# Optimization experiments

Measured on AMD Instinct MI355X. Metric: run time of the kernel, lower is better.

Reference implementation:

```python
import jax, jax.numpy as jnp
import numpy as np

B = 512
IN_CORES = 12      # input_eff_capsules = 3072/256
N_PRIM = 12        # num_primary_capsules
N_PAR = 10         # num_parent_capsules
RFPC = 4           # receptive fields per capsule = 256/64
RF = 64            # receptive field size
CAP = 256          # capsule size
P_CONN = 0.2


def setup_inputs() -> dict:
    key = jax.random.key(0)
    ks = jax.random.split(key, 16)
    x = jax.random.uniform(ks[0], (B, 32, 32, 3), dtype=jnp.float32)
    # sparse 0/1 routing tensors (fixed Bernoulli(p) connectivity, stored as float params)
    C1 = jax.random.bernoulli(ks[1], P_CONN, (IN_CORES, RFPC, N_PRIM, RFPC)).astype(jnp.float32)
    C_skip = jax.random.bernoulli(ks[2], P_CONN, (IN_CORES, RFPC, N_PAR, RFPC)).astype(jnp.float32)
    C2 = jax.random.bernoulli(ks[3], P_CONN, (N_PRIM, RFPC, N_PAR, RFPC)).astype(jnp.float32)
    # per-receptive-field linear weights of the capsule layers
    s = 1.0 / np.sqrt(RF)
    W1 = jax.random.normal(ks[4], (N_PRIM, RFPC, RF, RF), dtype=jnp.float32) * s
    b1 = jnp.zeros((N_PRIM, RFPC, RF), dtype=jnp.float32)
    W2 = jax.random.normal(ks[5], (N_PAR, RFPC, RF, RF), dtype=jnp.float32) * s
    b2 = jnp.zeros((N_PAR, RFPC, RF), dtype=jnp.float32)
    # reconstruction MLP: 2560 -> 5000 -> 4000 -> 3072
    Wr1 = jax.random.normal(ks[6], (2560, 5000), dtype=jnp.float32) * (1.0 / np.sqrt(2560))
    br1 = jnp.zeros((5000,), dtype=jnp.float32)
    Wr2 = jax.random.normal(ks[7], (5000, 4000), dtype=jnp.float32) * (1.0 / np.sqrt(5000))
    br2 = jnp.zeros((4000,), dtype=jnp.float32)
    Wr3 = jax.random.normal(ks[8], (4000, 3072), dtype=jnp.float32) * (1.0 / np.sqrt(4000))
    br3 = jnp.zeros((3072,), dtype=jnp.float32)
    return {"x": x, "C1": C1, "W1": W1, "b1": b1, "C_skip": C_skip,
            "C2": C2, "W2": W2, "b2": b2,
            "Wr1": Wr1, "br1": br1, "Wr2": Wr2, "br2": br2, "Wr3": Wr3, "br3": br3}


def _caps_layer(x_flat, C, W, b):
    # x_flat: (B, in_cores*RFPC*RF); C: (in_cores, RFPC, out_caps, RFPC)
    bsz = x_flat.shape[0]
    in_cores = C.shape[0]
    xr = x_flat.reshape(bsz, in_cores, RFPC, RF)
    routed = jnp.einsum('ijkl,bijm->bklm', C, xr)          # (B, out_caps, RFPC, RF)
    out = jax.nn.relu(jnp.einsum('bklm,klmn->bkln', routed, W) + b)
    return out.reshape(bsz, -1)


def reference(x, C1, W1, b1, C_skip, C2, W2, b2, Wr1, br1, Wr2, br2, Wr3, br3):
    bsz = x.shape[0]
    # spatial_block_reshape: pure reshapes -> flatten
    x_flat = x.reshape(bsz, -1)                             # (B, 3072)
    # primary capsule layer
    x_prim = _caps_layer(x_flat, C1, W1, b1)                # (B, 3072)
    # skip connection: sparse routing einsum input->parent
    xr = x_prim.reshape(bsz, IN_CORES, RFPC, RF)
    x_skip = jnp.einsum('ijkl,bijm->bklm', C_skip, xr).reshape(bsz, -1)  # (B, 2560)
    # parent capsule layer + skip
    x_sum = x_skip + _caps_layer(x_prim, C2, W2, b2)        # (B, 2560)
    # top-1 capsule mask by norm
    norms = jnp.linalg.norm(x_sum.reshape(bsz, N_PAR, CAP), axis=-1)  # (B, 10)
    active = jnp.argmax(norms, axis=-1)                     # (B,)
    cap_id = jnp.arange(N_PAR * CAP) // CAP                 # (2560,)
    mask = (cap_id[None, :] == active[:, None]).astype(x_sum.dtype)
    x_recon = mask * x_sum
    # reconstruction MLP
    h = jax.nn.relu(x_recon @ Wr1 + br1)
    h = jax.nn.relu(h @ Wr2 + br2)
    out = jax.nn.sigmoid(h @ Wr3 + br3)                     # (B, 3072)
    return (out, x_sum)
```

## Files before the change

kernel.cpp:

```cpp
#include <hip/hip_runtime.h>
#include <math.h>


#define BATCH 512
#define OUT0_SZ (512*3072)

#define KP1 2576
#define KP2 5136
#define KP3 4112
#define LD_XREC 2576
#define LD_H1 5136
#define LD_H2 4112
#define LDP2 4224
#define LDP3 3200
#define SPLITK 4

typedef __attribute__((ext_vector_type(8))) short short8;
typedef __attribute__((ext_vector_type(4))) float f32x4;

__device__ inline unsigned short f2bf(float f) {
    union { float f; unsigned u; } v; v.f = f;
    unsigned r = v.u + 0x7fffu + ((v.u >> 16) & 1u);
    return (unsigned short)(r >> 16);
}
__device__ inline float bf2f(unsigned int hi16) {
    union { unsigned u; float f; } v; v.u = hi16 << 16; return v.f;
}

#define GLD16(g, l) __builtin_amdgcn_global_load_lds( \
    (const __attribute__((address_space(1))) unsigned int*)(g), \
    (__attribute__((address_space(3))) unsigned int*)(l), 16, 0, 0)

#define GUEST_SMEM 16640

#define CONV_PARAMS const float* __restrict__ cWr1, unsigned short* __restrict__ cWt1, \
    const float* __restrict__ cWr2, unsigned short* __restrict__ cWt2, \
    const float* __restrict__ cWr3, unsigned short* __restrict__ cWt3

__device__ void conv_guest(int t, char* smem, CONV_PARAMS)
{
    float* sh = (float*)smem;
    const float* W; unsigned short* Wt;
    int Kr, Nr, Kp, ktiles, rem;
    if (t < 3200)      { W = cWr1; Wt = cWt1; Kr = 2560; Nr = 5000; Kp = KP1; ktiles = 40; rem = t; }
    else if (t < 8320) { W = cWr2; Wt = cWt2; Kr = 5000; Nr = 4000; Kp = KP2; ktiles = 80; rem = t - 3200; }
    else               { W = cWr3; Wt = cWt3; Kr = 4000; Nr = 3072; Kp = KP3; ktiles = 64; rem = t - 8320; }
    int k0 = (rem % ktiles) * 64;
    int n0 = (rem / ktiles) * 64;
    int tid = threadIdx.x;

    {
        int kr = tid >> 4;
        int nc = (tid & 15) * 4;
        #pragma unroll
        for (int p = 0; p < 4; ++p) {
            int k = k0 + kr + p * 16;
            float4 v = make_float4(0.f, 0.f, 0.f, 0.f);
            if (k < Kr) {
                if (n0 + nc + 3 < Nr) {
                    v = *(const float4*)&W[(size_t)k * Nr + n0 + nc];
                } else {
                    float tmp[4] = {0.f, 0.f, 0.f, 0.f};
                    #pragma unroll
                    for (int j = 0; j < 4; ++j)
                        if (n0 + nc + j < Nr) tmp[j] = W[(size_t)k * Nr + n0 + nc + j];
                    v = make_float4(tmp[0], tmp[1], tmp[2], tmp[3]);
                }
            }
            float* row = &sh[(kr + p * 16) * 65 + nc];
            row[0] = v.x; row[1] = v.y; row[2] = v.z; row[3] = v.w;
        }
    }
    __syncthreads();
    {
        int nr = tid >> 2;
        int kc = (tid & 3) * 16;
        unsigned int u[8];
        #pragma unroll
        for (int j = 0; j < 8; ++j) {
            float v0 = sh[(kc + 2 * j)     * 65 + nr];
            float v1 = sh[(kc + 2 * j + 1) * 65 + nr];
            u[j] = (unsigned int)f2bf(v0) | ((unsigned int)f2bf(v1) << 16);
        }
        unsigned int* dst = (unsigned int*)&Wt[(size_t)(n0 + nr) * Kp + k0 + kc];
        *(uint4*)(dst)     = make_uint4(u[0], u[1], u[2], u[3]);
        *(uint4*)(dst + 4) = make_uint4(u[4], u[5], u[6], u[7]);
    }
}

__global__ __launch_bounds__(256) void conv_small(
    const float* __restrict__ W1, unsigned short* __restrict__ W1t,
    const float* __restrict__ W2, unsigned short* __restrict__ W2t)
{
    __shared__ __align__(16) float sh[64 * 65];
    int bid = blockIdx.x;
    const float* W; unsigned short* Wt;
    if (bid < 48) { W = W1 + (size_t)bid * 4096; Wt = W1t + (size_t)bid * 4096; }
    else          { W = W2 + (size_t)(bid - 48) * 4096; Wt = W2t + (size_t)(bid - 48) * 4096; }
    int tid = threadIdx.x;
    int kr = tid >> 4, nc = (tid & 15) * 4;
    #pragma unroll
    for (int p = 0; p < 4; ++p) {
        float4 v = *(const float4*)&W[(size_t)(kr + p * 16) * 64 + nc];
        float* row = &sh[(kr + p * 16) * 65 + nc];
        row[0] = v.x; row[1] = v.y; row[2] = v.z; row[3] = v.w;
    }
    __syncthreads();
    int nr = tid >> 2, kc = (tid & 3) * 16;
    unsigned int u[8];
    #pragma unroll
    for (int j = 0; j < 8; ++j) {
        float v0 = sh[(kc + 2 * j)     * 65 + nr];
        float v1 = sh[(kc + 2 * j + 1) * 65 + nr];
        u[j] = (unsigned int)f2bf(v0) | ((unsigned int)f2bf(v1) << 16);
    }
    unsigned int* dst = (unsigned int*)&Wt[(size_t)nr * 64 + kc];
    *(uint4*)(dst)     = make_uint4(u[0], u[1], u[2], u[3]);
    *(uint4*)(dst + 4) = make_uint4(u[4], u[5], u[6], u[7]);
}

__global__ __launch_bounds__(256) void caps_gemm1_f(
    const float* __restrict__ x, const float* __restrict__ C1,
    const unsigned short* __restrict__ W1t, const float* __restrict__ b1,
    unsigned short* __restrict__ xp, int hostBlocks, int guestBase,
    CONV_PARAMS)
{
    __shared__ __align__(16) char smem[27840];
    if ((int)blockIdx.x >= hostBlocks) {
        conv_guest(guestBase + blockIdx.x - hostBlocks, smem, cWr1, cWt1, cWr2, cWt2, cWr3, cWt3);
        return;
    }
    unsigned short* As = (unsigned short*)smem;
    unsigned short* Bs = (unsigned short*)(smem + 18432);
    float* Csh = (float*)(smem + 27648);

    int kl = blockIdx.x % 48;
    int bm = (blockIdx.x / 48) * 128;
    int tid = threadIdx.x;
    int w = tid >> 6, lane = tid & 63, q = lane >> 4, r16 = lane & 15;
    int wm = (w >> 1) * 64, wn = (w & 1) * 32;

    if (tid < 48) Csh[tid] = C1[tid * 48 + kl];
    {
        const uint4* src = (const uint4*)(W1t + (size_t)kl * 4096);
        #pragma unroll
        for (int p = 0; p < 2; ++p) {
            int c = tid + p * 256;
            int row = c >> 3, cq = c & 7;
            *(uint4*)&Bs[row * 72 + cq * 8] = src[c];
        }
    }
    __syncthreads();

    int arow = tid >> 1, ah = (tid & 1) * 32;
    float accp[32];
    #pragma unroll
    for (int i = 0; i < 32; ++i) accp[i] = 0.f;
    const float* xrow = x + (size_t)(bm + arow) * 3072 + ah;
    for (int ij = 0; ij < 48; ++ij) {
        float c = Csh[ij];
        if (c != 0.f) {
            const float4* p4 = (const float4*)(xrow + ij * 64);
            #pragma unroll
            for (int cc = 0; cc < 8; ++cc) {
                float4 v = p4[cc];
                accp[cc * 4 + 0] = fmaf(c, v.x, accp[cc * 4 + 0]);
                accp[cc * 4 + 1] = fmaf(c, v.y, accp[cc * 4 + 1]);
                accp[cc * 4 + 2] = fmaf(c, v.z, accp[cc * 4 + 2]);
                accp[cc * 4 + 3] = fmaf(c, v.w, accp[cc * 4 + 3]);
            }
        }
    }
    {
        unsigned short* dst = &As[arow * 72 + ah];
        #pragma unroll
        for (int cc = 0; cc < 4; ++cc) {
            unsigned int u[4];
            #pragma unroll
            for (int j = 0; j < 4; ++j)
                u[j] = (unsigned int)f2bf(accp[cc * 8 + 2 * j]) |
                       ((unsigned int)f2bf(accp[cc * 8 + 2 * j + 1]) << 16);
            *(uint4*)&dst[cc * 8] = make_uint4(u[0], u[1], u[2], u[3]);
        }
    }
    __syncthreads();

    f32x4 acc[4][2];
    #pragma unroll
    for (int i = 0; i < 4; ++i)
        #pragma unroll
        for (int j = 0; j < 2; ++j) acc[i][j] = (f32x4)0.f;
    #pragma unroll
    for (int ks = 0; ks < 2; ++ks) {
        short8 a[4], b[2];
        #pragma unroll
        for (int mt = 0; mt < 4; ++mt)
            a[mt] = *(const short8*)&As[(wm + mt * 16 + r16) * 72 + ks * 32 + q * 8];
        #pragma unroll
        for (int nt = 0; nt < 2; ++nt)
            b[nt] = *(const short8*)&Bs[(wn + nt * 16 + r16) * 72 + ks * 32 + q * 8];
        #pragma unroll
        for (int mt = 0; mt < 4; ++mt)
            #pragma unroll
            for (int nt = 0; nt < 2; ++nt)
                acc[mt][nt] = __builtin_amdgcn_mfma_f32_16x16x32_bf16(a[mt], b[nt], acc[mt][nt], 0, 0, 0);
    }

    #pragma unroll
    for (int mt = 0; mt < 4; ++mt) {
        #pragma unroll
        for (int nt = 0; nt < 2; ++nt) {
            int n = wn + nt * 16 + r16;
            float bv = b1[kl * 64 + n];
            #pragma unroll
            for (int reg = 0; reg < 4; ++reg) {
                int row = bm + wm + mt * 16 + q * 4 + reg;
                xp[(size_t)row * 3072 + kl * 64 + n] = f2bf(fmaxf(acc[mt][nt][reg] + bv, 0.f));
            }
        }
    }
}

__global__ __launch_bounds__(256) void caps_gemm2_f(
    const unsigned short* __restrict__ xp, const float* __restrict__ Cs,
    const float* __restrict__ C2, const unsigned short* __restrict__ W2t,
    const float* __restrict__ b2, float* __restrict__ xsum,
    float* __restrict__ part8, int hostBlocks, int guestBase,
    CONV_PARAMS)
{
    __shared__ __align__(16) char smem[28032];
    if ((int)blockIdx.x >= hostBlocks) {
        conv_guest(guestBase + blockIdx.x - hostBlocks, smem, cWr1, cWt1, cWr2, cWt2, cWr3, cWt3);
        return;
    }
    unsigned short* As = (unsigned short*)smem;
    unsigned short* Bs = (unsigned short*)(smem + 18432);
    float* C2sh = (float*)(smem + 27648);
    float* Cssh = (float*)(smem + 27840);

    int kl = blockIdx.x % 40;
    int bm = (blockIdx.x / 40) * 128;
    int tid = threadIdx.x;
    int w = tid >> 6, lane = tid & 63, q = lane >> 4, r16 = lane & 15;
    int wm = (w >> 1) * 64, wn = (w & 1) * 32;
    int half = w & 1;

    if (tid < 48) { C2sh[tid] = C2[tid * 40 + kl]; Cssh[tid] = Cs[tid * 40 + kl]; }
    {
        const uint4* src = (const uint4*)(W2t + (size_t)kl * 4096);
        #pragma unroll
        for (int p = 0; p < 2; ++p) {
            int c = tid + p * 256;
            int row = c >> 3, cq = c & 7;
            *(uint4*)&Bs[row * 72 + cq * 8] = src[c];
        }
    }
    __syncthreads();

    int arow = tid >> 1, ah = (tid & 1) * 32;
    float accp[32], skp[32];
    #pragma unroll
    for (int i = 0; i < 32; ++i) { accp[i] = 0.f; skp[i] = 0.f; }
    const unsigned short* xprow = xp + (size_t)(bm + arow) * 3072 + ah;
    for (int ij = 0; ij < 48; ++ij) {
        float c2 = C2sh[ij], cs = Cssh[ij];
        if (c2 != 0.f || cs != 0.f) {
            const uint4* p4 = (const uint4*)(xprow + ij * 64);
            #pragma unroll
            for (int cc = 0; cc < 4; ++cc) {
                uint4 v = p4[cc];
                unsigned int uu[4] = {v.x, v.y, v.z, v.w};
                #pragma unroll
                for (int j = 0; j < 4; ++j) {
                    float lo = bf2f(uu[j] & 0xffffu);
                    float hi = bf2f(uu[j] >> 16);
                    int idx = cc * 8 + 2 * j;
                    accp[idx]     = fmaf(c2, lo, accp[idx]);
                    accp[idx + 1] = fmaf(c2, hi, accp[idx + 1]);
                    skp[idx]      = fmaf(cs, lo, skp[idx]);
                    skp[idx + 1]  = fmaf(cs, hi, skp[idx + 1]);
                }
            }
        }
    }
    {
        unsigned short* dst = &As[arow * 72 + ah];
        #pragma unroll
        for (int cc = 0; cc < 4; ++cc) {
            unsigned int u[4];
            #pragma unroll
            for (int j = 0; j < 4; ++j)
                u[j] = (unsigned int)f2bf(accp[cc * 8 + 2 * j]) |
                       ((unsigned int)f2bf(accp[cc * 8 + 2 * j + 1]) << 16);
            *(uint4*)&dst[cc * 8] = make_uint4(u[0], u[1], u[2], u[3]);
        }
        float* sx = xsum + (size_t)(bm + arow) * 2560 + kl * 64 + ah;
        #pragma unroll
        for (int cc = 0; cc < 8; ++cc)
            *(float4*)&sx[cc * 4] = make_float4(skp[cc*4], skp[cc*4+1], skp[cc*4+2], skp[cc*4+3]);
    }
    __syncthreads();

    f32x4 acc[4][2];
    #pragma unroll
    for (int i = 0; i < 4; ++i)
        #pragma unroll
        for (int j = 0; j < 2; ++j) acc[i][j] = (f32x4)0.f;
    #pragma unroll
    for (int ks = 0; ks < 2; ++ks) {
        short8 a[4], b[2];
        #pragma unroll
        for (int mt = 0; mt < 4; ++mt)
            a[mt] = *(const short8*)&As[(wm + mt * 16 + r16) * 72 + ks * 32 + q * 8];
        #pragma unroll
        for (int nt = 0; nt < 2; ++nt)
            b[nt] = *(const short8*)&Bs[(wn + nt * 16 + r16) * 72 + ks * 32 + q * 8];
        #pragma unroll
        for (int mt = 0; mt < 4; ++mt)
            #pragma unroll
            for (int nt = 0; nt < 2; ++nt)
                acc[mt][nt] = __builtin_amdgcn_mfma_f32_16x16x32_bf16(a[mt], b[nt], acc[mt][nt], 0, 0, 0);
    }

    #pragma unroll
    for (int mt = 0; mt < 4; ++mt) {
        float sreg[4] = {0.f, 0.f, 0.f, 0.f};
        #pragma unroll
        for (int nt = 0; nt < 2; ++nt) {
            int n = wn + nt * 16 + r16;
            float bv = b2[kl * 64 + n];
            #pragma unroll
            for (int reg = 0; reg < 4; ++reg) {
                int lr = wm + mt * 16 + q * 4 + reg;
                size_t xi = (size_t)(bm + lr) * 2560 + kl * 64 + n;
                float v = xsum[xi] + fmaxf(acc[mt][nt][reg] + bv, 0.f);
                xsum[xi] = v;
                sreg[reg] += v * v;
            }
        }
        #pragma unroll
        for (int reg = 0; reg < 4; ++reg) {
            float s = sreg[reg];
            s += __shfl_xor(s, 1); s += __shfl_xor(s, 2);
            s += __shfl_xor(s, 4); s += __shfl_xor(s, 8);
            if (r16 == 0) {
                int row = bm + wm + mt * 16 + q * 4 + reg;
                part8[(size_t)row * 80 + kl * 2 + half] = s;
            }
        }
    }
}

__global__ __launch_bounds__(256) void mask_f(
    const float* __restrict__ xs, const float* __restrict__ part8,
    unsigned short* __restrict__ xrec, int* __restrict__ active,
    int hostBlocks, int guestBase, CONV_PARAMS)
{
    __shared__ __align__(16) char smem[GUEST_SMEM + 64];
    if ((int)blockIdx.x >= hostBlocks) {
        conv_guest(guestBase + blockIdx.x - hostBlocks, smem, cWr1, cWt1, cWr2, cWt2, cWr3, cWt3);
        return;
    }
    float* norms = (float*)smem;
    int* actp = (int*)(smem + 40);
    int b = blockIdx.x;
    int tid = threadIdx.x;
    if (tid < 10) {
        float s = 0.f;
        #pragma unroll
        for (int j = 0; j < 8; ++j) s += part8[(size_t)b * 80 + tid * 8 + j];
        norms[tid] = s;
    }
    __syncthreads();
    if (tid == 0) {
        int best = 0; float bn = -1.f;
        #pragma unroll
        for (int k = 0; k < 10; ++k)
            if (norms[k] > bn) { bn = norms[k]; best = k; }
        *actp = best;
        active[b] = best;
    }
    __syncthreads();
    int act = *actp;
    int idx = act * 256 + tid;
    xrec[(size_t)b * LD_XREC + idx] = f2bf(xs[(size_t)b * 2560 + idx]);
}

__global__ __launch_bounds__(256) void bucket_f(
    const int* __restrict__ active, int* __restrict__ perm,
    int4* __restrict__ slots, int hostBlocks, int guestBase, CONV_PARAMS)
{
    __shared__ __align__(16) char smem[GUEST_SMEM + 128];
    if ((int)blockIdx.x >= hostBlocks) {
        conv_guest(guestBase + blockIdx.x - hostBlocks, smem, cWr1, cWt1, cWr2, cWt2, cWr3, cWt3);
        return;
    }
    int* cnt = (int*)smem;
    int* pos = cnt + 10;
    int tid = threadIdx.x;
    if (tid < 10) cnt[tid] = 0;
    __syncthreads();
    int a0 = active[tid], a1 = active[tid + 256];
    atomicAdd(&cnt[a0], 1);
    atomicAdd(&cnt[a1], 1);
    __syncthreads();
    if (tid == 0) {
        int o = 0, s = 0;
        for (int g = 0; g < 10; ++g) {
            pos[g] = o;
            int mg = cnt[g];
            for (int t0 = 0; t0 < mg; t0 += 64)
                slots[s++] = make_int4(g, o + t0, min(64, mg - t0), 0);
            o += mg;
        }
        for (; s < 18; ++s) slots[s] = make_int4(0, 0, 0, 0);
    }
    __syncthreads();
    int r0 = atomicAdd(&pos[a0], 1);
    perm[r0] = tid;
    int r1 = atomicAdd(&pos[a1], 1);
    perm[r1] = tid + 256;
}

__global__ __launch_bounds__(256) void gemm_l1_f(
    const unsigned short* __restrict__ xrec, const int* __restrict__ perm,
    const int4* __restrict__ slots, const unsigned short* __restrict__ Wt1,
    const float* __restrict__ br1, unsigned short* __restrict__ h1,
    int hostBlocks, int guestBase, CONV_PARAMS)
{
    __shared__ __align__(16) char smem[GUEST_SMEM];
    if ((int)blockIdx.x >= hostBlocks) {
        conv_guest(guestBase + blockIdx.x - hostBlocks, smem, cWr1, cWt1, cWr2, cWt2, cWr3, cWt3);
        return;
    }
    unsigned short* As = (unsigned short*)smem;
    unsigned short* Bs = (unsigned short*)(smem + 4096);
    int* rows = (int*)(smem + 12288);

    int sy = blockIdx.x % 18;
    int bn = (blockIdx.x / 18) * 128;
    int4 s = slots[sy];
    if (s.z == 0) return;
    int g = s.x, mstart = s.y, mval = s.z;
    int tid = threadIdx.x;

    if (tid < 64) rows[tid] = perm[mstart + min(tid, mval - 1)];
    __syncthreads();

    int w = tid >> 6, lane = tid & 63;
    int wm = (w >> 1) * 32, wn = (w & 1) * 64;
    int q = lane >> 4, r16 = lane & 15;
    int srow = tid >> 2, skq = tid & 3;

    f32x4 acc[2][4];
    #pragma unroll
    for (int i = 0; i < 2; ++i)
        #pragma unroll
        for (int j = 0; j < 4; ++j) acc[i][j] = (f32x4)0.f;

    int arow = rows[srow];
    const unsigned short* ga = xrec + (size_t)arow * LD_XREC + g * 256 + skq * 8;
    const unsigned short* gb = Wt1 + (size_t)(bn + srow) * KP1 + g * 256 + skq * 8;

    for (int kk = 0; kk < 256; kk += 32) {
        GLD16(ga + kk, &As[tid * 8]);
        GLD16(gb + kk, &Bs[tid * 8]);
        GLD16(gb + kk + (size_t)64 * KP1, &Bs[(tid + 256) * 8]);
        __syncthreads();

        short8 a[2], b[4];
        #pragma unroll
        for (int mt = 0; mt < 2; ++mt)
            a[mt] = *(const short8*)&As[(wm + mt * 16 + r16) * 32 + q * 8];
        #pragma unroll
        for (int nt = 0; nt < 4; ++nt)
            b[nt] = *(const short8*)&Bs[(wn + nt * 16 + r16) * 32 + q * 8];
        #pragma unroll
        for (int mt = 0; mt < 2; ++mt)
            #pragma unroll
            for (int nt = 0; nt < 4; ++nt)
                acc[mt][nt] = __builtin_amdgcn_mfma_f32_16x16x32_bf16(a[mt], b[nt], acc[mt][nt], 0, 0, 0);
        __syncthreads();
    }

    #pragma unroll
    for (int mt = 0; mt < 2; ++mt) {
        #pragma unroll
        for (int nt = 0; nt < 4; ++nt) {
            int n = bn + wn + nt * 16 + r16;
            float bv = (n < 5000) ? br1[n] : 0.f;
            #pragma unroll
            for (int reg = 0; reg < 4; ++reg) {
                int lm = wm + mt * 16 + q * 4 + reg;
                if (lm < mval)
                    h1[(size_t)(mstart + lm) * LD_H1 + n] =
                        f2bf(fmaxf(acc[mt][nt][reg] + bv, 0.f));
            }
        }
    }
}

__global__ __launch_bounds__(256) void gemm_splitk_f(
    const unsigned short* __restrict__ A, int ldA,
    const unsigned short* __restrict__ Bt, int ldB,
    float* __restrict__ P, int ldP, int Np, int kper, int nbx,
    int hostBlocks, int guestBase, CONV_PARAMS)
{
    __shared__ __align__(16) char smem[GUEST_SMEM];
    if ((int)blockIdx.x >= hostBlocks) {
        conv_guest(guestBase + blockIdx.x - hostBlocks, smem, cWr1, cWt1, cWr2, cWt2, cWr3, cWt3);
        return;
    }
    unsigned short* As = (unsigned short*)smem;
    unsigned short* Bs = (unsigned short*)(smem + 4096);

    int tid = threadIdx.x;
    int bid = blockIdx.x;
    int bn = (bid % nbx) * 128;
    int bm = ((bid / nbx) & 7) * 64;
    int z  = bid / (nbx * 8);
    int kz = z * kper;

    int w = tid >> 6, lane = tid & 63;
    int wm = (w >> 1) * 32, wn = (w & 1) * 64;
    int q = lane >> 4, r16 = lane & 15;
    int srow = tid >> 2, skq = tid & 3;

    f32x4 acc[2][4];
    #pragma unroll
    for (int i = 0; i < 2; ++i)
        #pragma unroll
        for (int j = 0; j < 4; ++j) acc[i][j] = (f32x4)0.f;

    for (int kk = 0; kk < kper; kk += 32) {
        int k0 = kz + kk;
        const unsigned short* ga = A + (size_t)(bm + srow) * ldA + k0 + skq * 8;
        GLD16(ga, &As[tid * 8]);
        const unsigned short* gb = Bt + (size_t)(bn + srow) * ldB + k0 + skq * 8;
        GLD16(gb, &Bs[tid * 8]);
        GLD16(gb + (size_t)64 * ldB, &Bs[(tid + 256) * 8]);
        __syncthreads();

        short8 a[2], b[4];
        #pragma unroll
        for (int mt = 0; mt < 2; ++mt)
            a[mt] = *(const short8*)&As[(wm + mt * 16 + r16) * 32 + q * 8];
        #pragma unroll
        for (int nt = 0; nt < 4; ++nt)
            b[nt] = *(const short8*)&Bs[(wn + nt * 16 + r16) * 32 + q * 8];
        #pragma unroll
        for (int mt = 0; mt < 2; ++mt)
            #pragma unroll
            for (int nt = 0; nt < 4; ++nt)
                acc[mt][nt] = __builtin_amdgcn_mfma_f32_16x16x32_bf16(a[mt], b[nt], acc[mt][nt], 0, 0, 0);
        __syncthreads();
    }

    float* Pz = P + (size_t)z * 512 * ldP;
    #pragma unroll
    for (int mt = 0; mt < 2; ++mt) {
        #pragma unroll
        for (int nt = 0; nt < 4; ++nt) {
            int cn = bn + wn + nt * 16 + r16;
            #pragma unroll
            for (int reg = 0; reg < 4; ++reg) {
                int cm = bm + wm + mt * 16 + q * 4 + reg;
                Pz[(size_t)cm * ldP + cn] = acc[mt][nt][reg];
            }
        }
    }
}

template<int MODE>
__global__ __launch_bounds__(256) void combine_f(
    const float* __restrict__ P, int ldP, const float* __restrict__ bias,
    void* __restrict__ out, int ldO, int Np, int N_real,
    const int* __restrict__ perm, int hostBlocks, int guestBase, CONV_PARAMS)
{
    __shared__ __align__(16) char smem[GUEST_SMEM];
    if ((int)blockIdx.x >= hostBlocks) {
        conv_guest(guestBase + blockIdx.x - hostBlocks, smem, cWr1, cWt1, cWr2, cWt2, cWr3, cWt3);
        return;
    }
    int gid = blockIdx.x * 256 + threadIdx.x;
    int n0 = (gid * 4) % Np;
    int m  = (gid * 4) / Np;
    size_t MN = (size_t)512 * ldP;
    const float* p = P + (size_t)m * ldP + n0;
    f32x4 s = *(const f32x4*)p;
    s += *(const f32x4*)(p + MN);
    s += *(const f32x4*)(p + 2 * MN);
    s += *(const f32x4*)(p + 3 * MN);
    f32x4 bv = (n0 < N_real) ? *(const f32x4*)(bias + n0) : (f32x4)0.f;
    s += bv;
    if (MODE == 0) {
        unsigned int lo = (unsigned int)f2bf(fmaxf(s[0], 0.f)) | ((unsigned int)f2bf(fmaxf(s[1], 0.f)) << 16);
        unsigned int hi = (unsigned int)f2bf(fmaxf(s[2], 0.f)) | ((unsigned int)f2bf(fmaxf(s[3], 0.f)) << 16);
        *(uint2*)((unsigned short*)out + (size_t)m * ldO + n0) = make_uint2(lo, hi);
    } else {
        int row = perm[m];
        f32x4 v;
        v[0] = 1.f / (1.f + expf(-s[0]));
        v[1] = 1.f / (1.f + expf(-s[1]));
        v[2] = 1.f / (1.f + expf(-s[2]));
        v[3] = 1.f / (1.f + expf(-s[3]));
        *(f32x4*)((float*)out + (size_t)row * ldO + n0) = v;
    }
}

extern "C" void kernel_launch(void* const* d_in, const int* in_sizes, int n_in,
                              void* d_out, int out_size, void* d_ws, size_t ws_size,
                              hipStream_t stream) {
    const float* x   = (const float*)d_in[0];
    const float* C1  = (const float*)d_in[1];
    const float* W1  = (const float*)d_in[2];
    const float* b1  = (const float*)d_in[3];
    const float* Cs  = (const float*)d_in[4];
    const float* C2  = (const float*)d_in[5];
    const float* W2  = (const float*)d_in[6];
    const float* b2  = (const float*)d_in[7];
    const float* Wr1 = (const float*)d_in[8];
    const float* br1 = (const float*)d_in[9];
    const float* Wr2 = (const float*)d_in[10];
    const float* br2 = (const float*)d_in[11];
    const float* Wr3 = (const float*)d_in[12];
    const float* br3 = (const float*)d_in[13];

    float* out = (float*)d_out;
    float* out0     = out;
    float* xsum_out = out + OUT0_SZ;

    char* base = (char*)d_ws;
    unsigned short* xrec = (unsigned short*)(base);
    unsigned short* h1   = (unsigned short*)(base +   2637824);
    unsigned short* h2   = (unsigned short*)(base +   7897088);
    unsigned short* Wt1  = (unsigned short*)(base +  12107776);
    unsigned short* Wt2  = (unsigned short*)(base +  38486016);
    unsigned short* Wt3  = (unsigned short*)(base +  80560128);
    float*          Pbuf = (float*)(base + 105824256);
    unsigned short* xp   = (unsigned short*)(base + 140427264);
    unsigned short* W1t  = (unsigned short*)(base + 143572992);
    unsigned short* W2t  = (unsigned short*)(base + 143966208);
    float*          part8= (float*)(base + 144293888);
    int*  active = (int*)(base + 144457728);
    int*  perm   = active + 512;
    int4* slots  = (int4*)(perm + 512);

    #define CARGS Wr1, Wt1, Wr2, Wt2, Wr3, Wt3

    conv_small<<<88, 256, 0, stream>>>(W1, W1t, W2, W2t);

    caps_gemm1_f<<<192 + 1600, 256, 0, stream>>>(x, C1, W1t, b1, xp, 192, 0, CARGS);
    caps_gemm2_f<<<160 + 1600, 256, 0, stream>>>(xp, Cs, C2, W2t, b2, xsum_out, part8, 160, 1600, CARGS);
    mask_f<<<512 + 1300, 256, 0, stream>>>(xsum_out, part8, xrec, active, 512, 3200, CARGS);
    bucket_f<<<1 + 1300, 256, 0, stream>>>(active, perm, slots, 1, 4500, CARGS);

    gemm_l1_f<<<720 + 2520, 256, 0, stream>>>(xrec, perm, slots, Wt1, br1, h1, 720, 5800, CARGS);

    gemm_splitk_f<<<1024 + 2000, 256, 0, stream>>>(h1, LD_H1, Wt2, KP2, Pbuf, LDP2, 4096, 5120 / SPLITK, 32, 1024, 8320, CARGS);
    combine_f<0><<<2048 + 1072, 256, 0, stream>>>(Pbuf, LDP2, br2, h2, LD_H2, 4096, 4000, nullptr, 2048, 10320, CARGS);

    gemm_splitk_f<<<768, 256, 0, stream>>>(h2, LD_H2, Wt3, KP3, Pbuf, LDP3, 3072, 4096 / SPLITK, 24, 768, 0, CARGS);
    combine_f<1><<<1536, 256, 0, stream>>>(Pbuf, LDP3, br3, out0, 3072, 3072, 3072, perm, 1536, 0, CARGS);
}
```

Measured before the change: 392.0 us.

## Double-buffer LDS in MLP GEMMs and drop LDS from weight-conversion guests

The sparse first-layer GEMM and the split-K GEMM now use two LDS buffers. The next k-tile's global-to-LDS loads are issued before computing on the current tile, which removes one barrier per iteration and overlaps loads with MFMA work. The weight-conversion guest code and conv_small no longer transpose through shared memory. Each thread instead reads 16 strided column elements straight from global memory, so kernels that are not GEMMs need little LDS, which may raise occupancy. The catch is that these strided global reads are poorly coalesced, and the doubled GEMM LDS footprint may lower occupancy.

New measurement: 413.8 us. +5.6%, slower.

```diff
diff --git a/kernel.cpp b/kernel.cpp
--- a/kernel.cpp
+++ b/kernel.cpp
@@ -31,15 +31,12 @@
     (const __attribute__((address_space(1))) unsigned int*)(g), \
     (__attribute__((address_space(3))) unsigned int*)(l), 16, 0, 0)
 
-#define GUEST_SMEM 16640
-
 #define CONV_PARAMS const float* __restrict__ cWr1, unsigned short* __restrict__ cWt1, \
     const float* __restrict__ cWr2, unsigned short* __restrict__ cWt2, \
     const float* __restrict__ cWr3, unsigned short* __restrict__ cWt3
 
-__device__ void conv_guest(int t, char* smem, CONV_PARAMS)
-{
-    float* sh = (float*)smem;
+__device__ void conv_guest(int t, CONV_PARAMS)
+{
     const float* W; unsigned short* Wt;
     int Kr, Nr, Kp, ktiles, rem;
     if (t < 3200)      { W = cWr1; Wt = cWt1; Kr = 2560; Nr = 5000; Kp = KP1; ktiles = 40; rem = t; }
@@ -49,71 +46,50 @@
     int n0 = (rem / ktiles) * 64;
     int tid = threadIdx.x;
 
-    {
-        int kr = tid >> 4;
-        int nc = (tid & 15) * 4;
-        #pragma unroll
-        for (int p = 0; p < 4; ++p) {
-            int k = k0 + kr + p * 16;
-            float4 v = make_float4(0.f, 0.f, 0.f, 0.f);
-            if (k < Kr) {
-                if (n0 + nc + 3 < Nr) {
-                    v = *(const float4*)&W[(size_t)k * Nr + n0 + nc];
-                } else {
-                    float tmp[4] = {0.f, 0.f, 0.f, 0.f};
-                    #pragma unroll
-                    for (int j = 0; j < 4; ++j)
-                        if (n0 + nc + j < Nr) tmp[j] = W[(size_t)k * Nr + n0 + nc + j];
-                    v = make_float4(tmp[0], tmp[1], tmp[2], tmp[3]);
-                }
-            }
-            float* row = &sh[(kr + p * 16) * 65 + nc];
-            row[0] = v.x; row[1] = v.y; row[2] = v.z; row[3] = v.w;
-        }
-    }
-    __syncthreads();
-    {
-        int nr = tid >> 2;
-        int kc = (tid & 3) * 16;
-        unsigned int u[8];
-        #pragma unroll
-        for (int j = 0; j < 8; ++j) {
-            float v0 = sh[(kc + 2 * j)     * 65 + nr];
-            float v1 = sh[(kc + 2 * j + 1) * 65 + nr];
-            u[j] = (unsigned int)f2bf(v0) | ((unsigned int)f2bf(v1) << 16);
-        }
-        unsigned int* dst = (unsigned int*)&Wt[(size_t)(n0 + nr) * Kp + k0 + kc];
-        *(uint4*)(dst)     = make_uint4(u[0], u[1], u[2], u[3]);
-        *(uint4*)(dst + 4) = make_uint4(u[4], u[5], u[6], u[7]);
-    }
+    int nr = tid >> 2;
+    int kc = (tid & 3) * 16;
+    int n = n0 + nr;
+
+    float v[16];
+    if (n < Nr) {
+        const float* col = W + (size_t)(k0 + kc) * Nr + n;
+        #pragma unroll
+        for (int i = 0; i < 16; ++i) {
+            int k = k0 + kc + i;
+            v[i] = (k < Kr) ? col[(size_t)i * Nr] : 0.f;
+        }
+    } else {
+        #pragma unroll
+        for (int i = 0; i < 16; ++i) v[i] = 0.f;
+    }
+    unsigned int u[8];
+    #pragma unroll
+    for (int j = 0; j < 8; ++j)
+        u[j] = (unsigned int)f2bf(v[2 * j]) | ((unsigned int)f2bf(v[2 * j + 1]) << 16);
+    unsigned int* dst = (unsigned int*)&Wt[(size_t)n * Kp + k0 + kc];
+    *(uint4*)(dst)     = make_uint4(u[0], u[1], u[2], u[3]);
+    *(uint4*)(dst + 4) = make_uint4(u[4], u[5], u[6], u[7]);
 }
 
 __global__ __launch_bounds__(256) void conv_small(
     const float* __restrict__ W1, unsigned short* __restrict__ W1t,
     const float* __restrict__ W2, unsigned short* __restrict__ W2t)
 {
-    __shared__ __align__(16) float sh[64 * 65];
     int bid = blockIdx.x;
     const float* W; unsigned short* Wt;
     if (bid < 48) { W = W1 + (size_t)bid * 4096; Wt = W1t + (size_t)bid * 4096; }
     else          { W = W2 + (size_t)(bid - 48) * 4096; Wt = W2t + (size_t)(bid - 48) * 4096; }
     int tid = threadIdx.x;
-    int kr = tid >> 4, nc = (tid & 15) * 4;
-    #pragma unroll
-    for (int p = 0; p < 4; ++p) {
-        float4 v = *(const float4*)&W[(size_t)(kr + p * 16) * 64 + nc];
-        float* row = &sh[(kr + p * 16) * 65 + nc];
-        row[0] = v.x; row[1] = v.y; row[2] = v.z; row[3] = v.w;
-    }
-    __syncthreads();
-    int nr = tid >> 2, kc = (tid & 3) * 16;
+    int nr = tid >> 2;
+    int kc = (tid & 3) * 16;
+    float v[16];
+    #pragma unroll
+    for (int i = 0; i < 16; ++i)
+        v[i] = W[(size_t)(kc + i) * 64 + nr];
     unsigned int u[8];
     #pragma unroll
-    for (int j = 0; j < 8; ++j) {
-        float v0 = sh[(kc + 2 * j)     * 65 + nr];
-        float v1 = sh[(kc + 2 * j + 1) * 65 + nr];
-        u[j] = (unsigned int)f2bf(v0) | ((unsigned int)f2bf(v1) << 16);
-    }
+    for (int j = 0; j < 8; ++j)
+        u[j] = (unsigned int)f2bf(v[2 * j]) | ((unsigned int)f2bf(v[2 * j + 1]) << 16);
     unsigned int* dst = (unsigned int*)&Wt[(size_t)nr * 64 + kc];
     *(uint4*)(dst)     = make_uint4(u[0], u[1], u[2], u[3]);
     *(uint4*)(dst + 4) = make_uint4(u[4], u[5], u[6], u[7]);
@@ -125,11 +101,11 @@
     unsigned short* __restrict__ xp, int hostBlocks, int guestBase,
     CONV_PARAMS)
 {
+    if ((int)blockIdx.x >= hostBlocks) {
+        conv_guest(guestBase + blockIdx.x - hostBlocks, cWr1, cWt1, cWr2, cWt2, cWr3, cWt3);
+        return;
+    }
     __shared__ __align__(16) char smem[27840];
-    if ((int)blockIdx.x >= hostBlocks) {
-        conv_guest(guestBase + blockIdx.x - hostBlocks, smem, cWr1, cWt1, cWr2, cWt2, cWr3, cWt3);
-        return;
-    }
     unsigned short* As = (unsigned short*)smem;
     unsigned short* Bs = (unsigned short*)(smem + 18432);
     float* Csh = (float*)(smem + 27648);
@@ -228,11 +204,11 @@
     float* __restrict__ part8, int hostBlocks, int guestBase,
     CONV_PARAMS)
 {
+    if ((int)blockIdx.x >= hostBlocks) {
+        conv_guest(guestBase + blockIdx.x - hostBlocks, cWr1, cWt1, cWr2, cWt2, cWr3, cWt3);
+        return;
+    }
     __shared__ __align__(16) char smem[28032];
-    if ((int)blockIdx.x >= hostBlocks) {
-        conv_guest(guestBase + blockIdx.x - hostBlocks, smem, cWr1, cWt1, cWr2, cWt2, cWr3, cWt3);
-        return;
-    }
     unsigned short* As = (unsigned short*)smem;
     unsigned short* Bs = (unsigned short*)(smem + 18432);
     float* C2sh = (float*)(smem + 27648);
@@ -356,13 +332,12 @@
     unsigned short* __restrict__ xrec, int* __restrict__ active,
     int hostBlocks, int guestBase, CONV_PARAMS)
 {
-    __shared__ __align__(16) char smem[GUEST_SMEM + 64];
     if ((int)blockIdx.x >= hostBlocks) {
-        conv_guest(guestBase + blockIdx.x - hostBlocks, smem, cWr1, cWt1, cWr2, cWt2, cWr3, cWt3);
+        conv_guest(guestBase + blockIdx.x - hostBlocks, cWr1, cWt1, cWr2, cWt2, cWr3, cWt3);
         return;
     }
-    float* norms = (float*)smem;
-    int* actp = (int*)(smem + 40);
+    __shared__ float norms[10];
+    __shared__ int act_sh;
     int b = blockIdx.x;
     int tid = threadIdx.x;
     if (tid < 10) {
@@ -377,11 +352,11 @@
         #pragma unroll
         for (int k = 0; k < 10; ++k)
             if (norms[k] > bn) { bn = norms[k]; best = k; }
-        *actp = best;
+        act_sh = best;
         active[b] = best;
     }
     __syncthreads();
-    int act = *actp;
+    int act = act_sh;
     int idx = act * 256 + tid;
     xrec[(size_t)b * LD_XREC + idx] = f2bf(xs[(size_t)b * 2560 + idx]);
 }
@@ -390,13 +365,11 @@
     const int* __restrict__ active, int* __restrict__ perm,
     int4* __restrict__ slots, int hostBlocks, int guestBase, CONV_PARAMS)
 {
-    __shared__ __align__(16) char smem[GUEST_SMEM + 128];
     if ((int)blockIdx.x >= hostBlocks) {
-        conv_guest(guestBase + blockIdx.x - hostBlocks, smem, cWr1, cWt1, cWr2, cWt2, cWr3, cWt3);
+        conv_guest(guestBase + blockIdx.x - hostBlocks, cWr1, cWt1, cWr2, cWt2, cWr3, cWt3);
         return;
     }
-    int* cnt = (int*)smem;
-    int* pos = cnt + 10;
+    __shared__ int cnt[10], pos[10];
     int tid = threadIdx.x;
     if (tid < 10) cnt[tid] = 0;
     __syncthreads();
@@ -428,14 +401,13 @@
     const float* __restrict__ br1, unsigned short* __restrict__ h1,
     int hostBlocks, int guestBase, CONV_PARAMS)
 {
-    __shared__ __align__(16) char smem[GUEST_SMEM];
     if ((int)blockIdx.x >= hostBlocks) {
-        conv_guest(guestBase + blockIdx.x - hostBlocks, smem, cWr1, cWt1, cWr2, cWt2, cWr3, cWt3);
+        conv_guest(guestBase + blockIdx.x - hostBlocks, cWr1, cWt1, cWr2, cWt2, cWr3, cWt3);
         return;
     }
-    unsigned short* As = (unsigned short*)smem;
-    unsigned short* Bs = (unsigned short*)(smem + 4096);
-    int* rows = (int*)(smem + 12288);
+    __shared__ __align__(16) unsigned short As[2][64 * 32];
+    __shared__ __align__(16) unsigned short Bs[2][128 * 32];
+    __shared__ int rows[64];
 
     int sy = blockIdx.x % 18;
     int bn = (blockIdx.x / 18) * 128;
@@ -461,26 +433,49 @@
     int arow = rows[srow];
     const unsigned short* ga = xrec + (size_t)arow * LD_XREC + g * 256 + skq * 8;
     const unsigned short* gb = Wt1 + (size_t)(bn + srow) * KP1 + g * 256 + skq * 8;
-
-    for (int kk = 0; kk < 256; kk += 32) {
-        GLD16(ga + kk, &As[tid * 8]);
-        GLD16(gb + kk, &Bs[tid * 8]);
-        GLD16(gb + kk + (size_t)64 * KP1, &Bs[(tid + 256) * 8]);
-        __syncthreads();
+    const unsigned short* gb2 = gb + (size_t)64 * KP1;
+
+    GLD16(ga, &As[0][tid * 8]);
+    GLD16(gb, &Bs[0][tid * 8]);
+    GLD16(gb2, &Bs[0][(tid + 256) * 8]);
+    __syncthreads();
+
+    int cur = 0;
+    #pragma unroll 1
+    for (int kk = 32; kk < 256; kk += 32) {
+        int nxt = cur ^ 1;
+        GLD16(ga + kk, &As[nxt][tid * 8]);
+        GLD16(gb + kk, &Bs[nxt][tid * 8]);
+        GLD16(gb2 + kk, &Bs[nxt][(tid + 256) * 8]);
 
         short8 a[2], b[4];
         #pragma unroll
         for (int mt = 0; mt < 2; ++mt)
-            a[mt] = *(const short8*)&As[(wm + mt * 16 + r16) * 32 + q * 8];
+            a[mt] = *(const short8*)&As[cur][(wm + mt * 16 + r16) * 32 + q * 8];
         #pragma unroll
         for (int nt = 0; nt < 4; ++nt)
-            b[nt] = *(const short8*)&Bs[(wn + nt * 16 + r16) * 32 + q * 8];
+            b[nt] = *(const short8*)&Bs[cur][(wn + nt * 16 + r16) * 32 + q * 8];
         #pragma unroll
         for (int mt = 0; mt < 2; ++mt)
             #pragma unroll
             for (int nt = 0; nt < 4; ++nt)
                 acc[mt][nt] = __builtin_amdgcn_mfma_f32_16x16x32_bf16(a[mt], b[nt], acc[mt][nt], 0, 0, 0);
         __syncthreads();
+        cur = nxt;
+    }
+    {
+        short8 a[2], b[4];
+        #pragma unroll
+        for (int mt = 0; mt < 2; ++mt)
+            a[mt] = *(const short8*)&As[cur][(wm + mt * 16 + r16) * 32 + q * 8];
+        #pragma unroll
+        for (int nt = 0; nt < 4; ++nt)
+            b[nt] = *(const short8*)&Bs[cur][(wn + nt * 16 + r16) * 32 + q * 8];
+        #pragma unroll
+        for (int mt = 0; mt < 2; ++mt)
+            #pragma unroll
+            for (int nt = 0; nt < 4; ++nt)
+                acc[mt][nt] = __builtin_amdgcn_mfma_f32_16x16x32_bf16(a[mt], b[nt], acc[mt][nt], 0, 0, 0);
     }
 
     #pragma unroll
@@ -506,13 +501,12 @@
     float* __restrict__ P, int ldP, int Np, int kper, int nbx,
     int hostBlocks, int guestBase, CONV_PARAMS)
 {
-    __shared__ __align__(16) char smem[GUEST_SMEM];
     if ((int)blockIdx.x >= hostBlocks) {
-        conv_guest(guestBase + blockIdx.x - hostBlocks, smem, cWr1, cWt1, cWr2, cWt2, cWr3, cWt3);
+        conv_guest(guestBase + blockIdx.x - hostBlocks, cWr1, cWt1, cWr2, cWt2, cWr3, cWt3);
         return;
     }
-    unsigned short* As = (unsigned short*)smem;
-    unsigned short* Bs = (unsigned short*)(smem + 4096);
+    __shared__ __align__(16) unsigned short As[2][64 * 32];
+    __shared__ __align__(16) unsigned short Bs[2][128 * 32];
 
     int tid = threadIdx.x;
     int bid = blockIdx.x;
@@ -532,28 +526,51 @@
         #pragma unroll
         for (int j = 0; j < 4; ++j) acc[i][j] = (f32x4)0.f;
 
-    for (int kk = 0; kk < kper; kk += 32) {
-        int k0 = kz + kk;
-        const unsigned short* ga = A + (size_t)(bm + srow) * ldA + k0 + skq * 8;
-        GLD16(ga, &As[tid * 8]);
-        const unsigned short* gb = Bt + (size_t)(bn + srow) * ldB + k0 + skq * 8;
-        GLD16(gb, &Bs[tid * 8]);
-        GLD16(gb + (size_t)64 * ldB, &Bs[(tid + 256) * 8]);
-        __syncthreads();
+    const unsigned short* ga  = A + (size_t)(bm + srow) * ldA + kz + skq * 8;
+    const unsigned short* gb  = Bt + (size_t)(bn + srow) * ldB + kz + skq * 8;
+    const unsigned short* gb2 = gb + (size_t)64 * ldB;
+
+    GLD16(ga, &As[0][tid * 8]);
+    GLD16(gb, &Bs[0][tid * 8]);
+    GLD16(gb2, &Bs[0][(tid + 256) * 8]);
+    __syncthreads();
+
+    int cur = 0;
+    #pragma unroll 1
+    for (int kk = 32; kk < kper; kk += 32) {
+        int nxt = cur ^ 1;
+        GLD16(ga + kk, &As[nxt][tid * 8]);
+        GLD16(gb + kk, &Bs[nxt][tid * 8]);
+        GLD16(gb2 + kk, &Bs[nxt][(tid + 256) * 8]);
 
         short8 a[2], b[4];
         #pragma unroll
         for (int mt = 0; mt < 2; ++mt)
-            a[mt] = *(const short8*)&As[(wm + mt * 16 + r16) * 32 + q * 8];
+            a[mt] = *(const short8*)&As[cur][(wm + mt * 16 + r16) * 32 + q * 8];
         #pragma unroll
         for (int nt = 0; nt < 4; ++nt)
-            b[nt] = *(const short8*)&Bs[(wn + nt * 16 + r16) * 32 + q * 8];
+            b[nt] = *(const short8*)&Bs[cur][(wn + nt * 16 + r16) * 32 + q * 8];
         #pragma unroll
         for (int mt = 0; mt < 2; ++mt)
             #pragma unroll
             for (int nt = 0; nt < 4; ++nt)
                 acc[mt][nt] = __builtin_amdgcn_mfma_f32_16x16x32_bf16(a[mt], b[nt], acc[mt][nt], 0, 0, 0);
         __syncthreads();
+        cur = nxt;
+    }
+    {
+        short8 a[2], b[4];
+        #pragma unroll
+        for (int mt = 0; mt < 2; ++mt)
+            a[mt] = *(const short8*)&As[cur][(wm + mt * 16 + r16) * 32 + q * 8];
+        #pragma unroll
+        for (int nt = 0; nt < 4; ++nt)
+            b[nt] = *(const short8*)&Bs[cur][(wn + nt * 16 + r16) * 32 + q * 8];
+        #pragma unroll
+        for (int mt = 0; mt < 2; ++mt)
+            #pragma unroll
+            for (int nt = 0; nt < 4; ++nt)
+                acc[mt][nt] = __builtin_amdgcn_mfma_f32_16x16x32_bf16(a[mt], b[nt], acc[mt][nt], 0, 0, 0);
     }
 
     float* Pz = P + (size_t)z * 512 * ldP;
@@ -577,9 +594,8 @@
     void* __restrict__ out, int ldO, int Np, int N_real,
     const int* __restrict__ perm, int hostBlocks, int guestBase, CONV_PARAMS)
 {
-    __shared__ __align__(16) char smem[GUEST_SMEM];
     if ((int)blockIdx.x >= hostBlocks) {
-        conv_guest(guestBase + blockIdx.x - hostBlocks, smem, cWr1, cWt1, cWr2, cWt2, cWr3, cWt3);
+        conv_guest(guestBase + blockIdx.x - hostBlocks, cWr1, cWt1, cWr2, cWt2, cWr3, cWt3);
         return;
     }
     int gid = blockIdx.x * 256 + threadIdx.x;
```
